# Kernel optimization log

Measured on AMD Instinct MI355X. Metric: run time of the kernel, lower is better.

## Reference

```python
import jax, jax.numpy as jnp
import numpy as np

D_MODEL = 1024
H = 16
D_K = D_MODEL // H
B = 2
S = 2048
NEG = -1e10


def setup_inputs() -> dict:
    key = jax.random.key(0)
    ks = jax.random.split(key, 12)
    sc = 1.0 / np.sqrt(D_MODEL)
    inp = {
        "q": jax.random.normal(ks[0], (B, S, D_MODEL), jnp.float32),
        "k": jax.random.normal(ks[1], (B, S, D_MODEL), jnp.float32),
        "v": jax.random.normal(ks[2], (B, S, D_MODEL), jnp.float32),
        # causal mask, broadcast over batch and heads
        "mask": jnp.tril(jnp.ones((S, S), jnp.int32))[None, None, :, :],
        "w_q": jax.random.normal(ks[3], (D_MODEL, D_MODEL), jnp.float32) * sc,
        "b_q": jax.random.normal(ks[4], (D_MODEL,), jnp.float32) * sc,
        "w_k": jax.random.normal(ks[5], (D_MODEL, D_MODEL), jnp.float32) * sc,
        "b_k": jax.random.normal(ks[6], (D_MODEL,), jnp.float32) * sc,
        "w_v": jax.random.normal(ks[7], (D_MODEL, D_MODEL), jnp.float32) * sc,
        "b_v": jax.random.normal(ks[8], (D_MODEL,), jnp.float32) * sc,
        "w_o": jax.random.normal(ks[9], (D_MODEL, D_MODEL), jnp.float32) * sc,
        "b_o": jax.random.normal(ks[10], (D_MODEL,), jnp.float32) * sc,
    }
    return inp


def _split_heads(x):
    # [B, S, D] -> [B, H, S, d_k]
    b, s, _ = x.shape
    return x.reshape(b, s, H, D_K).transpose(0, 2, 1, 3)


def reference(q, k, v, mask, w_q, b_q, w_k, b_k, w_v, b_v, w_o, b_o):
    # Linear projections (torch Linear: x @ W.T + b)
    qh = _split_heads(q @ w_q.T + b_q)
    kh = _split_heads(k @ w_k.T + b_k)
    vh = _split_heads(v @ w_v.T + b_v)
    scale = 1.0 / jnp.sqrt(jnp.asarray(D_K, qh.dtype))
    scores = jnp.einsum("bhqd,bhkd->bhqk", qh, kh) * scale
    scores = jnp.where(mask == 0, jnp.asarray(NEG, scores.dtype), scores)
    attn = jax.nn.softmax(scores, axis=-1)  # dropout=0.0 -> identity
    x = jnp.einsum("bhqk,bhkd->bhqd", attn, vh)
    x = x.transpose(0, 2, 1, 3).reshape(q.shape[0], -1, H * D_K)
    out = x @ w_o.T + b_o
    return (out, attn)
```

## Files before the change

### kernel.cpp

```cpp
#include <hip/hip_runtime.h>
#include <hip/hip_bf16.h>

typedef unsigned short u16;
typedef unsigned int u32;
typedef __attribute__((ext_vector_type(8))) short bf16x8;
typedef __attribute__((ext_vector_type(4))) float f32x4;

#define SEQ 2048
#define DM 1024
#define NH 16
#define DKK 64
#define NB 2

__device__ __forceinline__ u16 f2bf(float f) {
  union { float f; u32 u; } x; x.f = f;
  u32 r = x.u + 0x7FFFu + ((x.u >> 16) & 1u);
  return (u16)(r >> 16);
}

__device__ __forceinline__ void gl_lds16(const void* g, void* l) {
  __builtin_amdgcn_global_load_lds(
      (const __attribute__((address_space(1))) u32*)g,
      (__attribute__((address_space(3))) u32*)l, 16, 0, 0);
}

#define MFMA16(a, b, c) __builtin_amdgcn_mfma_f32_16x16x32_bf16(a, b, c, 0, 0, 0)

__global__ __launch_bounds__(256) void cvt_bf16(const float* __restrict__ in,
                                                u16* __restrict__ out, int n4) {
  int i = blockIdx.x * 256 + threadIdx.x;
  if (i >= n4) return;
  float4 v = ((const float4*)in)[i];
  ushort4 o;
  o.x = f2bf(v.x); o.y = f2bf(v.y); o.z = f2bf(v.z); o.w = f2bf(v.w);
  ((ushort4*)out)[i] = o;
}

struct ProjArgs {
  const u16* A;
  const u16* W;
  const float* bias;
  u16* Y;
  float scale;
};

__global__ __launch_bounds__(256) void proj_qkv(ProjArgs a0, ProjArgs a1,
                                                ProjArgs a2) {
  ProjArgs pa = (blockIdx.z == 0) ? a0 : (blockIdx.z == 1) ? a1 : a2;
  const int K = DM;
  __shared__ __align__(16) u16 As[128 * 32];
  __shared__ __align__(16) u16 Bs[128 * 32];
  const int tid = threadIdx.x, lane = tid & 63, w = tid >> 6;
  const int lr = lane & 15, lg = lane >> 4;
  const int wr = w >> 1, wc = w & 1;
  const int r0 = blockIdx.x * 128, c0 = blockIdx.y * 128;
  f32x4 acc[4][4];
#pragma unroll
  for (int i = 0; i < 4; ++i)
#pragma unroll
    for (int j = 0; j < 4; ++j) acc[i][j] = (f32x4){0.f, 0.f, 0.f, 0.f};

  for (int k0 = 0; k0 < K; k0 += 32) {
    if (k0) __syncthreads();
#pragma unroll
    for (int c = 0; c < 2; ++c) {
      int idx = tid + 256 * c;
      int row = idx >> 2, seg = idx & 3;
      gl_lds16(pa.A + (size_t)(r0 + row) * K + k0 + seg * 8,
               (char*)As + idx * 16);
      gl_lds16(pa.W + (size_t)(c0 + row) * K + k0 + seg * 8,
               (char*)Bs + idx * 16);
    }
    __syncthreads();
    bf16x8 a[4], b[4];
#pragma unroll
    for (int i = 0; i < 4; ++i) {
      int row = wr * 64 + i * 16 + lr;
      a[i] = *(const bf16x8*)((const char*)As + row * 64 + lg * 16);
    }
#pragma unroll
    for (int j = 0; j < 4; ++j) {
      int row = wc * 64 + j * 16 + lr;
      b[j] = *(const bf16x8*)((const char*)Bs + row * 64 + lg * 16);
    }
#pragma unroll
    for (int i = 0; i < 4; ++i)
#pragma unroll
      for (int j = 0; j < 4; ++j) acc[i][j] = MFMA16(a[i], b[j], acc[i][j]);
  }
#pragma unroll
  for (int i = 0; i < 4; ++i)
#pragma unroll
    for (int j = 0; j < 4; ++j)
#pragma unroll
      for (int rg = 0; rg < 4; ++rg) {
        int row = r0 + wr * 64 + i * 16 + lg * 4 + rg;
        int col = c0 + wc * 64 + j * 16 + lr;
        float v = (acc[i][j][rg] + pa.bias[col]) * pa.scale;
        int bb = row >> 11, s = row & (SEQ - 1), h = col >> 6, d = col & 63;
        pa.Y[((size_t)(bb * NH + h) * SEQ + s) * DKK + d] = f2bf(v);
      }
}

__global__ __launch_bounds__(256) void mm_out(const u16* __restrict__ A,
                                              const u16* __restrict__ W,
                                              const float* __restrict__ bias,
                                              float* __restrict__ Y) {
  const int K = DM;
  __shared__ __align__(16) u16 As[128 * 32];
  __shared__ __align__(16) u16 Bs[128 * 32];
  const int tid = threadIdx.x, lane = tid & 63, w = tid >> 6;
  const int lr = lane & 15, lg = lane >> 4;
  const int wr = w >> 1, wc = w & 1;
  const int r0 = blockIdx.x * 128, c0 = blockIdx.y * 128;
  f32x4 acc[4][4];
#pragma unroll
  for (int i = 0; i < 4; ++i)
#pragma unroll
    for (int j = 0; j < 4; ++j) acc[i][j] = (f32x4){0.f, 0.f, 0.f, 0.f};

  for (int k0 = 0; k0 < K; k0 += 32) {
    if (k0) __syncthreads();
#pragma unroll
    for (int c = 0; c < 2; ++c) {
      int idx = tid + 256 * c;
      int row = idx >> 2, seg = idx & 3;
      gl_lds16(A + (size_t)(r0 + row) * K + k0 + seg * 8, (char*)As + idx * 16);
      gl_lds16(W + (size_t)(c0 + row) * K + k0 + seg * 8, (char*)Bs + idx * 16);
    }
    __syncthreads();
    bf16x8 a[4], b[4];
#pragma unroll
    for (int i = 0; i < 4; ++i) {
      int row = wr * 64 + i * 16 + lr;
      a[i] = *(const bf16x8*)((const char*)As + row * 64 + lg * 16);
    }
#pragma unroll
    for (int j = 0; j < 4; ++j) {
      int row = wc * 64 + j * 16 + lr;
      b[j] = *(const bf16x8*)((const char*)Bs + row * 64 + lg * 16);
    }
#pragma unroll
    for (int i = 0; i < 4; ++i)
#pragma unroll
      for (int j = 0; j < 4; ++j) acc[i][j] = MFMA16(a[i], b[j], acc[i][j]);
  }
#pragma unroll
  for (int i = 0; i < 4; ++i)
#pragma unroll
    for (int j = 0; j < 4; ++j)
#pragma unroll
      for (int rg = 0; rg < 4; ++rg) {
        int row = r0 + wr * 64 + i * 16 + lg * 4 + rg;
        int col = c0 + wc * 64 + j * 16 + lr;
        Y[(size_t)row * DM + col] = acc[i][j][rg] + bias[col];
      }
}

__global__ __launch_bounds__(256) void transpose_v(const u16* __restrict__ Vh,
                                                   u16* __restrict__ Vt) {
  const int st = blockIdx.x, bh = blockIdx.y;
  const u16* src = Vh + ((size_t)bh * SEQ + st * 64) * DKK;
  u16* dst = Vt + (size_t)bh * DKK * SEQ + st * 64;
  __shared__ u16 T[64][68];
  const int tid = threadIdx.x;
#pragma unroll
  for (int c = 0; c < 4; ++c) {
    int idx = tid + 256 * c;
    int r = idx >> 4, seg = idx & 15;
    ushort4 v = *(const ushort4*)(src + r * 64 + seg * 4);
    *(ushort4*)&T[r][seg * 4] = v;
  }
  __syncthreads();
#pragma unroll
  for (int c = 0; c < 4; ++c) {
    int idx = tid + 256 * c;
    int d = idx >> 4, sseg = idx & 15;
    ushort4 o;
    o.x = T[sseg * 4 + 0][d]; o.y = T[sseg * 4 + 1][d];
    o.z = T[sseg * 4 + 2][d]; o.w = T[sseg * 4 + 3][d];
    *(ushort4*)(dst + (size_t)d * SEQ + sseg * 4) = o;
  }
}

__global__ __launch_bounds__(256) void flash_fwd(const u16* __restrict__ Qh,
                                                 const u16* __restrict__ Kh,
                                                 const u16* __restrict__ Vt,
                                                 u16* __restrict__ X,
                                                 float* __restrict__ linv) {
  const int qi = (int)gridDim.x - 1 - (int)blockIdx.x;
  const int bh = blockIdx.y;
  const int q0 = qi * 128;
  const u16* Qb = Qh + (size_t)bh * SEQ * DKK;
  const u16* Kb = Kh + (size_t)bh * SEQ * DKK;
  const u16* Vb = Vt + (size_t)bh * DKK * SEQ;
  const int tid = threadIdx.x, lane = tid & 63, w = tid >> 6;
  const int lr = lane & 15, lg = lane >> 4;

  __shared__ __align__(16) u16 Ks[64 * 64];
  __shared__ __align__(16) u16 Vs[64 * 64];
  __shared__ __align__(16) u16 Ps[128 * 64];

  bf16x8 frQ[2][2];
#pragma unroll
  for (int ri = 0; ri < 2; ++ri)
#pragma unroll
    for (int kc = 0; kc < 2; ++kc) {
      int r = q0 + w * 32 + ri * 16 + lr;
      frQ[ri][kc] = *(const bf16x8*)(Qb + (size_t)r * DKK + kc * 32 + lg * 8);
    }

  f32x4 accO[2][4];
  float rs[2][4];
#pragma unroll
  for (int ri = 0; ri < 2; ++ri) {
#pragma unroll
    for (int ci = 0; ci < 4; ++ci) accO[ri][ci] = (f32x4){0.f, 0.f, 0.f, 0.f};
#pragma unroll
    for (int rg = 0; rg < 4; ++rg) rs[ri][rg] = 0.f;
  }

  const int wmax = q0 + w * 32 + 31;
  const int nkv = (qi + 1) * 2;
  for (int j = 0; j < nkv; ++j) {
    const int kv0 = j * 64;
    if (j) __syncthreads();
#pragma unroll
    for (int c = 0; c < 2; ++c) {
      int idx = tid + 256 * c;
      int row = idx >> 3, sq = idx & 7;
      int seg = sq ^ (row & 7);
      gl_lds16(Kb + (size_t)(kv0 + row) * DKK + seg * 8, (char*)Ks + idx * 16);
      gl_lds16(Vb + (size_t)row * SEQ + kv0 + seg * 8, (char*)Vs + idx * 16);
    }
    __syncthreads();
    if (kv0 <= wmax) {
      f32x4 sf[2][4];
#pragma unroll
      for (int ci = 0; ci < 4; ++ci) {
        bf16x8 bK[2];
#pragma unroll
        for (int kc = 0; kc < 2; ++kc) {
          int row = ci * 16 + lr;
          int q = (kc * 4 + lg) ^ (row & 7);
          bK[kc] = *(const bf16x8*)((const char*)Ks + row * 128 + q * 16);
        }
#pragma unroll
        for (int ri = 0; ri < 2; ++ri) {
          f32x4 a = (f32x4){0.f, 0.f, 0.f, 0.f};
          a = MFMA16(frQ[ri][0], bK[0], a);
          a = MFMA16(frQ[ri][1], bK[1], a);
          sf[ri][ci] = a;
        }
      }
#pragma unroll
      for (int ri = 0; ri < 2; ++ri)
#pragma unroll
        for (int ci = 0; ci < 4; ++ci)
#pragma unroll
          for (int rg = 0; rg < 4; ++rg) {
            int rloc = w * 32 + ri * 16 + lg * 4 + rg;
            int rglob = q0 + rloc;
            int cglob = kv0 + ci * 16 + lr;
            float p = (cglob <= rglob) ? __expf(sf[ri][ci][rg]) : 0.f;
            rs[ri][rg] += p;
            int col = ci * 16 + lr;
            int byte = rloc * 128 + (((col >> 3) ^ (rloc & 7)) << 4) +
                       (col & 7) * 2;
            *(u16*)((char*)Ps + byte) = f2bf(p);
          }
#pragma unroll
      for (int kvc = 0; kvc < 2; ++kvc) {
        bf16x8 aP[2];
#pragma unroll
        for (int ri = 0; ri < 2; ++ri) {
          int row = w * 32 + ri * 16 + lr;
          int q = (kvc * 4 + lg) ^ (row & 7);
          aP[ri] = *(const bf16x8*)((const char*)Ps + row * 128 + q * 16);
        }
#pragma unroll
        for (int ci = 0; ci < 4; ++ci) {
          int row = ci * 16 + lr;
          int q = (kvc * 4 + lg) ^ (row & 7);
          bf16x8 bV = *(const bf16x8*)((const char*)Vs + row * 128 + q * 16);
#pragma unroll
          for (int ri = 0; ri < 2; ++ri)
            accO[ri][ci] = MFMA16(aP[ri], bV, accO[ri][ci]);
        }
      }
    }
  }
  const int b = bh >> 4, h = bh & (NH - 1);
  float inv_[2][4];
#pragma unroll
  for (int ri = 0; ri < 2; ++ri)
#pragma unroll
    for (int rg = 0; rg < 4; ++rg) {
      float v = rs[ri][rg];
      v += __shfl_xor(v, 1);
      v += __shfl_xor(v, 2);
      v += __shfl_xor(v, 4);
      v += __shfl_xor(v, 8);
      float iv = 1.f / v;
      inv_[ri][rg] = iv;
      int rglob = q0 + w * 32 + ri * 16 + lg * 4 + rg;
      if (lr == 0) linv[(size_t)bh * SEQ + rglob] = iv;
    }
#pragma unroll
  for (int ri = 0; ri < 2; ++ri)
#pragma unroll
    for (int ci = 0; ci < 4; ++ci)
#pragma unroll
      for (int rg = 0; rg < 4; ++rg) {
        int srow = q0 + w * 32 + ri * 16 + lg * 4 + rg;
        int col = h * DKK + ci * 16 + lr;
        X[((size_t)(b * SEQ + srow)) * DM + col] =
            f2bf(accO[ri][ci][rg] * inv_[ri][rg]);
      }
}

__global__ __launch_bounds__(256) void attn_mat(const u16* __restrict__ Qh,
                                                const u16* __restrict__ Kh,
                                                const float* __restrict__ linv,
                                                float* __restrict__ attn) {
  const int rt = blockIdx.x, ct = blockIdx.y, bh = blockIdx.z;
  float* out = attn + (size_t)bh * SEQ * SEQ;
  const int tid = threadIdx.x;
  if (ct > rt) {
    float4 z = {0.f, 0.f, 0.f, 0.f};
#pragma unroll
    for (int c = 0; c < 4; ++c) {
      int idx = tid + 256 * c;
      int row = idx >> 4, c4 = idx & 15;
      *(float4*)(out + (size_t)(rt * 64 + row) * SEQ + ct * 64 + c4 * 4) = z;
    }
    return;
  }
  const u16* Qb = Qh + (size_t)bh * SEQ * DKK;
  const u16* Kb = Kh + (size_t)bh * SEQ * DKK;
  __shared__ __align__(16) u16 Qs[64 * 64];
  __shared__ __align__(16) u16 Ks2[64 * 64];
  const int lane = tid & 63, w = tid >> 6, lr = lane & 15, lg = lane >> 4;
#pragma unroll
  for (int c = 0; c < 2; ++c) {
    int idx = tid + 256 * c;
    int row = idx >> 3, sq = idx & 7, seg = sq ^ (row & 7);
    gl_lds16(Qb + (size_t)(rt * 64 + row) * DKK + seg * 8,
             (char*)Qs + idx * 16);
    gl_lds16(Kb + (size_t)(ct * 64 + row) * DKK + seg * 8,
             (char*)Ks2 + idx * 16);
  }
  __syncthreads();
  bf16x8 aQ[2];
#pragma unroll
  for (int kc = 0; kc < 2; ++kc) {
    int row = w * 16 + lr;
    int q = (kc * 4 + lg) ^ (row & 7);
    aQ[kc] = *(const bf16x8*)((const char*)Qs + row * 128 + q * 16);
  }
  float lrow[4];
#pragma unroll
  for (int rg = 0; rg < 4; ++rg)
    lrow[rg] = linv[(size_t)bh * SEQ + rt * 64 + w * 16 + lg * 4 + rg];
  const bool full = (ct < rt);
#pragma unroll
  for (int ci = 0; ci < 4; ++ci) {
    bf16x8 bK[2];
#pragma unroll
    for (int kc = 0; kc < 2; ++kc) {
      int row = ci * 16 + lr;
      int q = (kc * 4 + lg) ^ (row & 7);
      bK[kc] = *(const bf16x8*)((const char*)Ks2 + row * 128 + q * 16);
    }
    f32x4 a = (f32x4){0.f, 0.f, 0.f, 0.f};
    a = MFMA16(aQ[0], bK[0], a);
    a = MFMA16(aQ[1], bK[1], a);
#pragma unroll
    for (int rg = 0; rg < 4; ++rg) {
      int row = rt * 64 + w * 16 + lg * 4 + rg;
      int col = ct * 64 + ci * 16 + lr;
      float v = (full || col <= row) ? __expf(a[rg]) * lrow[rg] : 0.f;
      out[(size_t)row * SEQ + col] = v;
    }
  }
}

extern "C" void kernel_launch(void* const* d_in, const int* in_sizes, int n_in,
                              void* d_out, int out_size, void* d_ws,
                              size_t ws_size, hipStream_t stream) {
  const float* q = (const float*)d_in[0];
  const float* k = (const float*)d_in[1];
  const float* v = (const float*)d_in[2];
  const float* w_q = (const float*)d_in[4];
  const float* b_q = (const float*)d_in[5];
  const float* w_k = (const float*)d_in[6];
  const float* b_k = (const float*)d_in[7];
  const float* w_v = (const float*)d_in[8];
  const float* b_v = (const float*)d_in[9];
  const float* w_o = (const float*)d_in[10];
  const float* b_o = (const float*)d_in[11];

  float* out = (float*)d_out;
  float* attn = out + (size_t)NB * SEQ * DM;

  const size_t MB = 1u << 20;
  char* ws = (char*)d_ws;
  u16* qb = (u16*)(ws);
  u16* kb = (u16*)(ws + 8 * MB);
  u16* vb = (u16*)(ws + 16 * MB);
  u16* Qh = (u16*)(ws + 24 * MB);
  u16* Kh = (u16*)(ws + 32 * MB);
  u16* Vh = (u16*)(ws + 40 * MB);
  u16* wqb = (u16*)(ws + 48 * MB);
  u16* wkb = (u16*)(ws + 50 * MB);
  u16* wvb = (u16*)(ws + 52 * MB);
  u16* wob = (u16*)(ws + 54 * MB);
  float* linv = (float*)(ws + 56 * MB);
  u16* Vt = qb;
  u16* X = vb;

  dim3 blk(256);
  const int n4_qkv = NB * SEQ * DM / 4;
  const int n4_w = DM * DM / 4;
  cvt_bf16<<<dim3((n4_qkv + 255) / 256), blk, 0, stream>>>(q, qb, n4_qkv);
  cvt_bf16<<<dim3((n4_qkv + 255) / 256), blk, 0, stream>>>(k, kb, n4_qkv);
  cvt_bf16<<<dim3((n4_qkv + 255) / 256), blk, 0, stream>>>(v, vb, n4_qkv);
  cvt_bf16<<<dim3((n4_w + 255) / 256), blk, 0, stream>>>(w_q, wqb, n4_w);
  cvt_bf16<<<dim3((n4_w + 255) / 256), blk, 0, stream>>>(w_k, wkb, n4_w);
  cvt_bf16<<<dim3((n4_w + 255) / 256), blk, 0, stream>>>(w_v, wvb, n4_w);
  cvt_bf16<<<dim3((n4_w + 255) / 256), blk, 0, stream>>>(w_o, wob, n4_w);

  ProjArgs aq = {qb, wqb, b_q, Qh, 0.125f};
  ProjArgs ak = {kb, wkb, b_k, Kh, 1.0f};
  ProjArgs av = {vb, wvb, b_v, Vh, 1.0f};
  proj_qkv<<<dim3(NB * SEQ / 128, DM / 128, 3), blk, 0, stream>>>(aq, ak, av);

  transpose_v<<<dim3(SEQ / 64, NB * NH), blk, 0, stream>>>(Vh, Vt);

  flash_fwd<<<dim3(SEQ / 128, NB * NH), blk, 0, stream>>>(Qh, Kh, Vt, X, linv);

  mm_out<<<dim3(NB * SEQ / 128, DM / 128), blk, 0, stream>>>(X, wob, b_o, out);

  attn_mat<<<dim3(SEQ / 64, SEQ / 64, NB * NH), blk, 0, stream>>>(Qh, Kh, linv,
                                                                  attn);
}
```

Before: 284.7 us.

## Double-buffer flash attention KV loads, swap MFMA operands, batch conversion launches

Merges the seven fp32-to-bf16 conversion launches into two batched kernels to cut launch overhead. In flash_fwd, K/V tiles are double-buffered so the next tile's global-to-LDS load overlaps compute, with a single barrier per iteration. QK^T is computed transposed (K as the A operand) so each lane holds four consecutive kv entries for one query row; P is then written to per-wave LDS as packed 8-byte stores and row sums need fewer shuffles. It also adds a block-index swizzle and s_setprio around the math. The costs are doubled K/V LDS use, which may lower occupancy, and an extra shuffle to redistribute the inverse row sums.

```diff
diff --git a/kernel.cpp b/kernel.cpp
--- a/kernel.cpp
+++ b/kernel.cpp
@@ -25,9 +25,35 @@
 }
 
 #define MFMA16(a, b, c) __builtin_amdgcn_mfma_f32_16x16x32_bf16(a, b, c, 0, 0, 0)
-
-__global__ __launch_bounds__(256) void cvt_bf16(const float* __restrict__ in,
-                                                u16* __restrict__ out, int n4) {
+#define VMCNT0() asm volatile("s_waitcnt vmcnt(0)" ::: "memory")
+#define SCHEDB() __builtin_amdgcn_sched_barrier(0)
+
+__global__ __launch_bounds__(256) void cvt3(const float* __restrict__ i0,
+                                            const float* __restrict__ i1,
+                                            const float* __restrict__ i2,
+                                            u16* o0, u16* o1, u16* o2, int n4) {
+  const float* in = (blockIdx.y == 0) ? i0 : (blockIdx.y == 1) ? i1 : i2;
+  u16* out = (blockIdx.y == 0) ? o0 : (blockIdx.y == 1) ? o1 : o2;
+  int i = blockIdx.x * 256 + threadIdx.x;
+  if (i >= n4) return;
+  float4 v = ((const float4*)in)[i];
+  ushort4 o;
+  o.x = f2bf(v.x); o.y = f2bf(v.y); o.z = f2bf(v.z); o.w = f2bf(v.w);
+  ((ushort4*)out)[i] = o;
+}
+
+__global__ __launch_bounds__(256) void cvt4(const float* __restrict__ i0,
+                                            const float* __restrict__ i1,
+                                            const float* __restrict__ i2,
+                                            const float* __restrict__ i3,
+                                            u16* o0, u16* o1, u16* o2, u16* o3,
+                                            int n4) {
+  const float* in = (blockIdx.y == 0) ? i0
+                    : (blockIdx.y == 1) ? i1
+                    : (blockIdx.y == 2) ? i2 : i3;
+  u16* out = (blockIdx.y == 0) ? o0
+             : (blockIdx.y == 1) ? o1
+             : (blockIdx.y == 2) ? o2 : o3;
   int i = blockIdx.x * 256 + threadIdx.x;
   if (i >= n4) return;
   float4 v = ((const float4*)in)[i];
@@ -188,8 +214,11 @@
                                                  const u16* __restrict__ Vt,
                                                  u16* __restrict__ X,
                                                  float* __restrict__ linv) {
-  const int qi = (int)gridDim.x - 1 - (int)blockIdx.x;
-  const int bh = blockIdx.y;
+  const int lin = (int)(blockIdx.y * gridDim.x + blockIdx.x);
+  const int nwg = (int)(gridDim.x * gridDim.y);
+  const int swz = (lin & 7) * (nwg >> 3) + (lin >> 3);
+  const int qi = (int)gridDim.x - 1 - (swz & 15);
+  const int bh = swz >> 4;
   const int q0 = qi * 128;
   const u16* Qb = Qh + (size_t)bh * SEQ * DKK;
   const u16* Kb = Kh + (size_t)bh * SEQ * DKK;
@@ -197,9 +226,9 @@
   const int tid = threadIdx.x, lane = tid & 63, w = tid >> 6;
   const int lr = lane & 15, lg = lane >> 4;
 
-  __shared__ __align__(16) u16 Ks[64 * 64];
-  __shared__ __align__(16) u16 Vs[64 * 64];
-  __shared__ __align__(16) u16 Ps[128 * 64];
+  __shared__ __align__(16) u16 Ks[2][64 * 64];
+  __shared__ __align__(16) u16 Vs[2][64 * 64];
+  __shared__ __align__(16) u16 Ps[4 * 32 * 64];
 
   bf16x8 frQ[2][2];
 #pragma unroll
@@ -211,101 +240,127 @@
     }
 
   f32x4 accO[2][4];
-  float rs[2][4];
-#pragma unroll
-  for (int ri = 0; ri < 2; ++ri) {
+  float rs[2] = {0.f, 0.f};
+#pragma unroll
+  for (int ri = 0; ri < 2; ++ri)
 #pragma unroll
     for (int ci = 0; ci < 4; ++ci) accO[ri][ci] = (f32x4){0.f, 0.f, 0.f, 0.f};
-#pragma unroll
-    for (int rg = 0; rg < 4; ++rg) rs[ri][rg] = 0.f;
-  }
 
   const int wmax = q0 + w * 32 + 31;
   const int nkv = (qi + 1) * 2;
-  for (int j = 0; j < nkv; ++j) {
+
+  auto stage = [&](int j, int buf) {
     const int kv0 = j * 64;
-    if (j) __syncthreads();
 #pragma unroll
     for (int c = 0; c < 2; ++c) {
       int idx = tid + 256 * c;
       int row = idx >> 3, sq = idx & 7;
       int seg = sq ^ (row & 7);
-      gl_lds16(Kb + (size_t)(kv0 + row) * DKK + seg * 8, (char*)Ks + idx * 16);
-      gl_lds16(Vb + (size_t)row * SEQ + kv0 + seg * 8, (char*)Vs + idx * 16);
-    }
-    __syncthreads();
+      gl_lds16(Kb + (size_t)(kv0 + row) * DKK + seg * 8,
+               (char*)Ks[buf] + idx * 16);
+      gl_lds16(Vb + (size_t)row * SEQ + kv0 + seg * 8,
+               (char*)Vs[buf] + idx * 16);
+    }
+  };
+
+  stage(0, 0);
+  VMCNT0();
+  __builtin_amdgcn_s_barrier();
+  SCHEDB();
+
+  for (int j = 0; j < nkv; ++j) {
+    const int buf = j & 1;
+    const int kv0 = j * 64;
+    if (j + 1 < nkv) stage(j + 1, buf ^ 1);
+
     if (kv0 <= wmax) {
-      f32x4 sf[2][4];
+      __builtin_amdgcn_s_setprio(1);
+      f32x4 sf[4][2];
 #pragma unroll
       for (int ci = 0; ci < 4; ++ci) {
-        bf16x8 bK[2];
+        bf16x8 aK[2];
 #pragma unroll
         for (int kc = 0; kc < 2; ++kc) {
           int row = ci * 16 + lr;
           int q = (kc * 4 + lg) ^ (row & 7);
-          bK[kc] = *(const bf16x8*)((const char*)Ks + row * 128 + q * 16);
+          aK[kc] = *(const bf16x8*)((const char*)Ks[buf] + row * 128 + q * 16);
         }
 #pragma unroll
         for (int ri = 0; ri < 2; ++ri) {
           f32x4 a = (f32x4){0.f, 0.f, 0.f, 0.f};
-          a = MFMA16(frQ[ri][0], bK[0], a);
-          a = MFMA16(frQ[ri][1], bK[1], a);
-          sf[ri][ci] = a;
+          a = MFMA16(aK[0], frQ[ri][0], a);
+          a = MFMA16(aK[1], frQ[ri][1], a);
+          sf[ci][ri] = a;
         }
       }
 #pragma unroll
-      for (int ri = 0; ri < 2; ++ri)
-#pragma unroll
-        for (int ci = 0; ci < 4; ++ci)
+      for (int ri = 0; ri < 2; ++ri) {
+        const int qglob = q0 + w * 32 + ri * 16 + lr;
+        const int qlrow = ri * 16 + lr;
+#pragma unroll
+        for (int ci = 0; ci < 4; ++ci) {
+          float p[4];
 #pragma unroll
           for (int rg = 0; rg < 4; ++rg) {
-            int rloc = w * 32 + ri * 16 + lg * 4 + rg;
-            int rglob = q0 + rloc;
-            int cglob = kv0 + ci * 16 + lr;
-            float p = (cglob <= rglob) ? __expf(sf[ri][ci][rg]) : 0.f;
-            rs[ri][rg] += p;
-            int col = ci * 16 + lr;
-            int byte = rloc * 128 + (((col >> 3) ^ (rloc & 7)) << 4) +
-                       (col & 7) * 2;
-            *(u16*)((char*)Ps + byte) = f2bf(p);
+            int kvglob = kv0 + ci * 16 + lg * 4 + rg;
+            p[rg] = (kvglob <= qglob) ? __expf(sf[ci][ri][rg]) : 0.f;
           }
+          rs[ri] += (p[0] + p[1]) + (p[2] + p[3]);
+          u32 lo = (u32)f2bf(p[0]) | ((u32)f2bf(p[1]) << 16);
+          u32 hi = (u32)f2bf(p[2]) | ((u32)f2bf(p[3]) << 16);
+          int c16 = (ci * 2 + (lg >> 1)) ^ (lr & 7);
+          char* dst = (char*)Ps + w * 4096 + qlrow * 128 + c16 * 16 +
+                      (lg & 1) * 8;
+          *(uint2*)dst = (uint2){lo, hi};
+        }
+      }
 #pragma unroll
       for (int kvc = 0; kvc < 2; ++kvc) {
         bf16x8 aP[2];
 #pragma unroll
         for (int ri = 0; ri < 2; ++ri) {
-          int row = w * 32 + ri * 16 + lr;
-          int q = (kvc * 4 + lg) ^ (row & 7);
-          aP[ri] = *(const bf16x8*)((const char*)Ps + row * 128 + q * 16);
+          int qlrow = ri * 16 + lr;
+          int c16 = (kvc * 4 + lg) ^ (lr & 7);
+          aP[ri] = *(const bf16x8*)((const char*)Ps + w * 4096 + qlrow * 128 +
+                                    c16 * 16);
         }
 #pragma unroll
         for (int ci = 0; ci < 4; ++ci) {
           int row = ci * 16 + lr;
-          int q = (kvc * 4 + lg) ^ (row & 7);
-          bf16x8 bV = *(const bf16x8*)((const char*)Vs + row * 128 + q * 16);
+          int q2 = (kvc * 4 + lg) ^ (row & 7);
+          bf16x8 bV =
+              *(const bf16x8*)((const char*)Vs[buf] + row * 128 + q2 * 16);
 #pragma unroll
           for (int ri = 0; ri < 2; ++ri)
             accO[ri][ci] = MFMA16(aP[ri], bV, accO[ri][ci]);
         }
       }
-    }
-  }
+      __builtin_amdgcn_s_setprio(0);
+    }
+    VMCNT0();
+    __builtin_amdgcn_s_barrier();
+    SCHEDB();
+  }
+
   const int b = bh >> 4, h = bh & (NH - 1);
+  float vinv[2];
+#pragma unroll
+  for (int ri = 0; ri < 2; ++ri) {
+    float v = rs[ri];
+    v += __shfl_xor(v, 16);
+    v += __shfl_xor(v, 32);
+    float iv = 1.f / v;
+    vinv[ri] = iv;
+    int qglob = q0 + w * 32 + ri * 16 + lr;
+    if (lg == 0) linv[(size_t)bh * SEQ + qglob] = iv;
+  }
   float inv_[2][4];
 #pragma unroll
   for (int ri = 0; ri < 2; ++ri)
 #pragma unroll
-    for (int rg = 0; rg < 4; ++rg) {
-      float v = rs[ri][rg];
-      v += __shfl_xor(v, 1);
-      v += __shfl_xor(v, 2);
-      v += __shfl_xor(v, 4);
-      v += __shfl_xor(v, 8);
-      float iv = 1.f / v;
-      inv_[ri][rg] = iv;
-      int rglob = q0 + w * 32 + ri * 16 + lg * 4 + rg;
-      if (lr == 0) linv[(size_t)bh * SEQ + rglob] = iv;
-    }
+    for (int rg = 0; rg < 4; ++rg)
+      inv_[ri][rg] = __shfl(vinv[ri], lg * 4 + rg);
+
 #pragma unroll
   for (int ri = 0; ri < 2; ++ri)
 #pragma unroll
@@ -422,13 +477,10 @@
   dim3 blk(256);
   const int n4_qkv = NB * SEQ * DM / 4;
   const int n4_w = DM * DM / 4;
-  cvt_bf16<<<dim3((n4_qkv + 255) / 256), blk, 0, stream>>>(q, qb, n4_qkv);
-  cvt_bf16<<<dim3((n4_qkv + 255) / 256), blk, 0, stream>>>(k, kb, n4_qkv);
-  cvt_bf16<<<dim3((n4_qkv + 255) / 256), blk, 0, stream>>>(v, vb, n4_qkv);
-  cvt_bf16<<<dim3((n4_w + 255) / 256), blk, 0, stream>>>(w_q, wqb, n4_w);
-  cvt_bf16<<<dim3((n4_w + 255) / 256), blk, 0, stream>>>(w_k, wkb, n4_w);
-  cvt_bf16<<<dim3((n4_w + 255) / 256), blk, 0, stream>>>(w_v, wvb, n4_w);
-  cvt_bf16<<<dim3((n4_w + 255) / 256), blk, 0, stream>>>(w_o, wob, n4_w);
+  cvt3<<<dim3((n4_qkv + 255) / 256, 3), blk, 0, stream>>>(q, k, v, qb, kb, vb,
+                                                          n4_qkv);
+  cvt4<<<dim3((n4_w + 255) / 256, 4), blk, 0, stream>>>(
+      w_q, w_k, w_v, w_o, wqb, wkb, wvb, wob, n4_w);
 
   ProjArgs aq = {qb, wqb, b_q, Qh, 0.125f};
   ProjArgs ak = {kb, wkb, b_k, Kh, 1.0f};
```

New measurement: 282.1 us. About the same (-0.9%).
